# Kernel optimization log

Hardware: AMD Instinct MI355X
Metric: run time of the kernel (lower is better)

Reference implementation:

```python
import jax, jax.numpy as jnp
import numpy as np

N = 2048        # number of entities
D = 2048        # entity_dimensionality
HEADS = 16
HD = D // HEADS  # per-head dim = 128
ROUNDS = 2
LAYERS = 2


def setup_inputs() -> dict:
    key = jax.random.key(0)
    ks = jax.random.split(key, 12)
    s = 1.0 / np.sqrt(D)  # keep activations O(1)
    inp = {
        "entities": jax.random.normal(ks[0], (N, D), jnp.float32),
        "Wq": jax.random.normal(ks[1], (D, D), jnp.float32) * s,
        "bq": jnp.zeros((D,), jnp.float32),
        "Wk": jax.random.normal(ks[2], (D, D), jnp.float32) * s,
        "bk": jnp.zeros((D,), jnp.float32),
        "Wv": jax.random.normal(ks[3], (D, D), jnp.float32) * s,
        "bv": jnp.zeros((D,), jnp.float32),
        "W0": jax.random.normal(ks[4], (D, D), jnp.float32) * s,
        "b0": jnp.zeros((D,), jnp.float32),
        "W1": jax.random.normal(ks[5], (D, D), jnp.float32) * s,
        "b1": jnp.zeros((D,), jnp.float32),
    }
    return inp


def _linear(x, W, b):
    # torch nn.Linear: y = x @ W.T + b
    return x @ W.T + b


def _split_heads(x):
    # [N, D] -> [H, N, hd]
    return x.reshape(N, HEADS, HD).transpose(1, 0, 2)


def reference(entities, Wq, bq, Wk, bk, Wv, bv, W0, b0, W1, b1):
    scale = 1.0 / np.sqrt(HD)
    for _ in range(ROUNDS):
        q = _split_heads(_linear(entities, Wq, bq))  # [H, N, hd]
        k = _split_heads(_linear(entities, Wk, bk))
        v = _split_heads(_linear(entities, Wv, bv))
        scores = jnp.einsum('hqd,hkd->hqk', q, k) * scale  # [H, N, N]
        attn = jax.nn.softmax(scores, axis=-1)
        o = jnp.einsum('hqk,hkd->hqd', attn, v)            # [H, N, hd]
        o = o.transpose(1, 0, 2).reshape(N, D)             # merge heads
        o = jax.nn.relu(_linear(o, W0, b0))
        o = jax.nn.relu(_linear(o, W1, b1))
        entities = entities + o  # residual=True
    return entities
```

## Files before the change

### kernel.cpp

```cpp
#include <hip/hip_runtime.h>
#include <stdint.h>

#define DIM   2048
#define NENT  2048
#define NHEAD 16
#define HD    128

typedef unsigned short u16;
typedef u16   u16x4  __attribute__((ext_vector_type(4)));
typedef u16   u16x8  __attribute__((ext_vector_type(8)));
typedef float f32x4  __attribute__((ext_vector_type(4)));
typedef float f32x16 __attribute__((ext_vector_type(16)));
typedef __bf16 bf16x8 __attribute__((ext_vector_type(8)));

#define MFMA16(a, b, c) __builtin_amdgcn_mfma_f32_16x16x32_bf16((a), (b), (c), 0, 0, 0)
#define MFMA32(a, b, c) __builtin_amdgcn_mfma_f32_32x32x16_bf16((a), (b), (c), 0, 0, 0)

#define SMUL 0.12751743f

__device__ __forceinline__ u16 f2b(float f) {
  union { float f; unsigned int u; } x; x.f = f;
  unsigned int r = x.u + 0x7FFFu + ((x.u >> 16) & 1u);
  return (u16)(r >> 16);
}
__device__ __forceinline__ float b2f(u16 b) {
  union { unsigned int u; float f; } x; x.u = ((unsigned int)b) << 16;
  return x.f;
}
__device__ __forceinline__ unsigned int cvtpk(float a, float b) {
  unsigned int r;
  asm("v_cvt_pk_bf16_f32 %0, %1, %2" : "=v"(r) : "v"(a), "v"(b));
  return r;
}
__device__ __forceinline__ float exp2_fast(float x) {
  float r;
  asm("v_exp_f32 %0, %1" : "=v"(r) : "v"(x));
  return r;
}

__device__ __forceinline__ void async16(const void* g, void* l) {
  __builtin_amdgcn_global_load_lds(
      (const __attribute__((address_space(1))) unsigned int*)(uintptr_t)g,
      (__attribute__((address_space(3))) unsigned int*)(uintptr_t)l, 16, 0, 0);
}

__global__ void __launch_bounds__(256) conv6_k(
    const float* __restrict__ s0, const float* __restrict__ s1,
    const float* __restrict__ s2, const float* __restrict__ s3,
    const float* __restrict__ s4, const float* __restrict__ s5,
    u16* __restrict__ d0, u16* __restrict__ d1, u16* __restrict__ d2,
    u16* __restrict__ d3, u16* __restrict__ d4, u16* __restrict__ d5) {
  int sel = blockIdx.y;
  const float* s = sel == 0 ? s0 : sel == 1 ? s1 : sel == 2 ? s2
                 : sel == 3 ? s3 : sel == 4 ? s4 : s5;
  u16* d = sel == 0 ? d0 : sel == 1 ? d1 : sel == 2 ? d2
         : sel == 3 ? d3 : sel == 4 ? d4 : d5;
  int i = blockIdx.x * 256 + threadIdx.x;
  float4 v = ((const float4*)s)[i];
  u16x4 o;
  o.x = f2b(v.x); o.y = f2b(v.y); o.z = f2b(v.z); o.w = f2b(v.w);
  *(u16x4*)(d + (size_t)i * 4) = o;
}

template <int MODE, int NT>
__device__ __forceinline__ void gemm128_body(
    const u16* __restrict__ A, const u16* __restrict__ Bw,
    const float* __restrict__ bias, u16* __restrict__ C,
    int brow0, int bcol0, int kbase, float oscale) {
  __shared__ u16 lA[128 * 64];
  __shared__ u16 lB[128 * 64];
  const int tid = threadIdx.x;
  const int lane = tid & 63, w = tid >> 6;
  const int wr = w >> 1, wc = w & 1;
  const int l15 = lane & 15;
  const int koff = (lane >> 4) * 8;
  const int swz = (l15 & 7) << 3;

  f32x4 acc[4][4];
#pragma unroll
  for (int m = 0; m < 4; m++)
#pragma unroll
    for (int n = 0; n < 4; n++) acc[m][n] = (f32x4)0.f;

  const int lr = w * 8 + (lane >> 3);
  const int scol = ((lane & 7) ^ (lr & 7)) * 8;

#pragma unroll 1
  for (int kt = 0; kt < NT; kt++) {
    const int colg = kbase + kt * 64 + scol;
#pragma unroll
    for (int i = 0; i < 4; i++) {
      async16(A + (size_t)(brow0 + i * 32 + lr) * DIM + colg,
              lA + i * 2048 + w * 512);
      async16(Bw + (size_t)(bcol0 + i * 32 + lr) * DIM + colg,
              lB + i * 2048 + w * 512);
    }
    __syncthreads();
#pragma unroll
    for (int kk = 0; kk < 2; kk++) {
      bf16x8 af[4], bfr[4];
#pragma unroll
      for (int m = 0; m < 4; m++)
        af[m] = *(const bf16x8*)(lA + (wr * 64 + m * 16 + l15) * 64 +
                                 ((kk * 32 + koff) ^ swz));
#pragma unroll
      for (int n = 0; n < 4; n++)
        bfr[n] = *(const bf16x8*)(lB + (wc * 64 + n * 16 + l15) * 64 +
                                  ((kk * 32 + koff) ^ swz));
#pragma unroll
      for (int m = 0; m < 4; m++)
#pragma unroll
        for (int n = 0; n < 4; n++)
          acc[m][n] = MFMA16(af[m], bfr[n], acc[m][n]);
    }
    __syncthreads();
  }

#pragma unroll
  for (int n = 0; n < 4; n++) {
    int col = bcol0 + wc * 64 + n * 16 + l15;
    float bv = (MODE == 0) ? bias[col] : 0.f;
#pragma unroll
    for (int m = 0; m < 4; m++) {
#pragma unroll
      for (int r = 0; r < 4; r++) {
        int row = brow0 + wr * 64 + m * 16 + (lane >> 4) * 4 + r;
        float val = acc[m][n][r] + bv;
        if (MODE == 0) val *= oscale;
        C[(size_t)row * DIM + col] = f2b(val);
      }
    }
  }
}

__global__ void __launch_bounds__(256, 3) gemm128_qkv_k(
    const u16* __restrict__ A,
    const u16* __restrict__ Bq, const u16* __restrict__ Bk, const u16* __restrict__ Bv,
    const float* __restrict__ bq, const float* __restrict__ bk, const float* __restrict__ bv,
    u16* __restrict__ q, u16* __restrict__ k, u16* __restrict__ v) {
  int x = blockIdx.x & 7;
  int j = blockIdx.x >> 3;
  int bn48 = x * 6 + j % 6;
  int bm = j / 6;
  int sel = bn48 >> 4, bnn = bn48 & 15;
  const u16* B = sel == 0 ? Bq : (sel == 1 ? Bk : Bv);
  const float* bias = sel == 0 ? bq : (sel == 1 ? bk : bv);
  u16* Cc = sel == 0 ? q : (sel == 1 ? k : v);
  gemm128_body<0, 32>(A, B, bias, Cc, bm * 128, bnn * 128, 0,
                      sel == 0 ? SMUL : 1.f);
}

__global__ void __launch_bounds__(256, 3) gemm128_sk_k(
    const u16* __restrict__ A, const u16* __restrict__ Bw,
    u16* __restrict__ p0, u16* __restrict__ p1) {
  int x = blockIdx.x & 7;
  int j = blockIdx.x >> 3;
  int bn = 2 * x + (j & 1);
  int sk = (j >> 1) & 1;
  int bm = j >> 2;
  u16* part = sk ? p1 : p0;
  gemm128_body<1, 16>(A, Bw, nullptr, part, bm * 128, bn * 128, sk * 1024, 1.f);
}

template <int RESID>
__global__ void __launch_bounds__(256) reduce2_k(
    const u16* __restrict__ p0, const u16* __restrict__ p1,
    const float* __restrict__ bias, const float* __restrict__ resid,
    float* __restrict__ outf, u16* __restrict__ outb) {
  int i = blockIdx.x * 256 + threadIdx.x;
  u16x8 a0 = ((const u16x8*)p0)[i];
  u16x8 a1 = ((const u16x8*)p1)[i];
  size_t base = (size_t)i * 8;
  int col = (int)(base & (DIM - 1));
  u16x8 ob;
  float of[8];
#pragma unroll
  for (int j = 0; j < 8; j++) {
    float s = b2f(a0[j]) + b2f(a1[j]) + bias[col + j];
    s = fmaxf(s, 0.f);
    if (RESID) {
      float o = resid[base + j] + s;
      of[j] = o;
      ob[j] = f2b(o);
    } else {
      ob[j] = f2b(s);
    }
  }
  *(u16x8*)(outb + base) = ob;
  if (RESID) {
#pragma unroll
    for (int j = 0; j < 8; j++) outf[base + j] = of[j];
  }
}

__global__ void __launch_bounds__(256) transpose_v_k(const u16* __restrict__ v,
                                                     u16* __restrict__ vt) {
  __shared__ u16 t[64][72];
  int h = blockIdx.z, nb = blockIdx.y, db = blockIdx.x;
  int tid = threadIdx.x;
  int r0 = tid >> 3, c0 = (tid & 7) * 8;
#pragma unroll
  for (int p = 0; p < 2; p++) {
    int r = r0 + p * 32;
    const u16* src = v + (size_t)(nb * 64 + r) * DIM + h * HD + db * 64 + c0;
    u16x8 x = *(const u16x8*)src;
#pragma unroll
    for (int j = 0; j < 8; j++) t[r][c0 + j] = x[j];
  }
  __syncthreads();
#pragma unroll
  for (int p = 0; p < 2; p++) {
    int rr = r0 + p * 32;
    u16x8 x;
#pragma unroll
    for (int j = 0; j < 8; j++) x[j] = t[c0 + j][rr];
    *(u16x8*)(vt + (size_t)h * HD * NENT + (size_t)(db * 64 + rr) * NENT + nb * 64 + c0) = x;
  }
}

__global__ void __launch_bounds__(256, 2) attn_k(
    const u16* __restrict__ q, const u16* __restrict__ kmat,
    const u16* __restrict__ vt, u16* __restrict__ oz0, u16* __restrict__ oz1,
    float* __restrict__ ml) {
  const int h = blockIdx.x, qb = blockIdx.y, kvs = blockIdx.z;
  u16* __restrict__ oz = kvs ? oz1 : oz0;
  __shared__ u16 lK[2][64 * 128];
  __shared__ u16 lV[2][128 * 64];
  const int tid = threadIdx.x, lane = tid & 63, w = tid >> 6;
  const int l31 = lane & 31, hl = lane >> 5;
  const int r4 = lane >> 4, r8 = lane >> 3;
  const int c16e = (lane & 15) * 8, c8e = (lane & 7) * 8;
  const int swz = (l31 & 7) << 3;
  const u16* vhead = vt + (size_t)h * HD * NENT;
  const int kv0 = kvs * (NENT / 2);

  const int qrow = qb * 128 + w * 32 + l31;
  const u16* qptr = q + (size_t)qrow * DIM + h * HD + hl * 8;
  bf16x8 qf[8];
#pragma unroll
  for (int ks = 0; ks < 8; ks++)
    qf[ks] = *(const bf16x8*)(qptr + ks * 16);

  auto stageKV = [&](int kt, int buf) {
    const size_t krow0 = (size_t)kv0 + kt * 64;
#pragma unroll
    for (int c = 0; c < 4; c++) {
      int ch = w * 4 + c;
      int krow = ch * 4 + r4;
      async16(kmat + (krow0 + krow) * DIM + h * HD + (c16e ^ ((krow & 7) << 3)),
              lK[buf] + ch * 512);
      int vrow = ch * 8 + r8;
      async16(vhead + (size_t)vrow * NENT + krow0 + (c8e ^ ((r8 & 7) << 3)),
              lV[buf] + ch * 512);
    }
  };

  f32x16 Oacc[4];
#pragma unroll
  for (int dt = 0; dt < 4; dt++) Oacc[dt] = (f32x16)0.f;
  float m_i = -1e30f, l_i = 0.f;

  stageKV(0, 0);
  int cur = 0;

#pragma unroll 1
  for (int kt = 0; kt < NENT / 2 / 64; kt++) {
    __syncthreads();
    if (kt + 1 < NENT / 2 / 64) stageKV(kt + 1, cur ^ 1);
    const u16* Kc = lK[cur];
    const u16* Vc = lV[cur];

    f32x16 sA = (f32x16)0.f, sB = (f32x16)0.f;
#pragma unroll
    for (int ks = 0; ks < 8; ks++) {
      bf16x8 a0 = *(const bf16x8*)(Kc + l31 * 128 + ((ks * 16 + hl * 8) ^ swz));
      sA = MFMA32(a0, qf[ks], sA);
      bf16x8 a1 = *(const bf16x8*)(Kc + (32 + l31) * 128 + ((ks * 16 + hl * 8) ^ swz));
      sB = MFMA32(a1, qf[ks], sB);
    }

    float pmax = sA[0];
#pragma unroll
    for (int i = 1; i < 16; i++) pmax = fmaxf(pmax, sA[i]);
#pragma unroll
    for (int i = 0; i < 16; i++) pmax = fmaxf(pmax, sB[i]);
    pmax = fmaxf(pmax, __shfl_xor(pmax, 32));
    bool resc = __any(pmax > m_i + 8.f);
    float corr = 1.f;
    if (resc) {
      float mn = fmaxf(m_i, pmax);
      corr = exp2_fast(m_i - mn);
      m_i = mn;
    }
    float ls = 0.f;
#pragma unroll
    for (int i = 0; i < 16; i++) { sA[i] = exp2_fast(sA[i] - m_i); ls += sA[i]; }
#pragma unroll
    for (int i = 0; i < 16; i++) { sB[i] = exp2_fast(sB[i] - m_i); ls += sB[i]; }
    l_i = l_i * corr + ls;
    if (resc) {
#pragma unroll
      for (int r = 0; r < 16; r++) {
        int qo = hl * 4 + (r & 3) + 8 * (r >> 2);
        float cr = __shfl(corr, qo);
        Oacc[0][r] *= cr; Oacc[1][r] *= cr; Oacc[2][r] *= cr; Oacc[3][r] *= cr;
      }
    }

#pragma unroll
    for (int ks = 0; ks < 4; ks++) {
      const f32x16& p = (ks < 2) ? sA : sB;
      const int E = ((2 * ks) & 3) * 4;
      const int Od = ((2 * ks + 1) & 3) * 4;
      unsigned int e0 = cvtpk(p[E + 0], p[E + 1]);
      unsigned int e1 = cvtpk(p[E + 2], p[E + 3]);
      unsigned int o0 = cvtpk(p[Od + 0], p[Od + 1]);
      unsigned int o1 = cvtpk(p[Od + 2], p[Od + 3]);
      asm volatile("v_permlane32_swap_b32 %0, %1" : "+v"(e0), "+v"(o0));
      asm volatile("v_permlane32_swap_b32 %0, %1" : "+v"(e1), "+v"(o1));
      union { unsigned int u[4]; bf16x8 v; } pk;
      pk.u[0] = e0; pk.u[1] = e1; pk.u[2] = o0; pk.u[3] = o1;
#pragma unroll
      for (int dt = 0; dt < 4; dt++) {
        bf16x8 b = *(const bf16x8*)(Vc + (dt * 32 + l31) * 64 +
                                    ((ks * 16 + hl * 8) ^ swz));
        Oacc[dt] = MFMA32(pk.v, b, Oacc[dt]);
      }
    }
    cur ^= 1;
  }

  float lt = l_i + __shfl_xor(l_i, 32);
  if (hl == 0) {
    float* mlp = ml + ((size_t)(kvs * NHEAD + h) * NENT + qrow) * 2;
    mlp[0] = m_i;
    mlp[1] = lt;
  }
#pragma unroll
  for (int r = 0; r < 16; r++) {
    int row = qb * 128 + w * 32 + hl * 4 + (r & 3) + 8 * (r >> 2);
#pragma unroll
    for (int dt = 0; dt < 4; dt++)
      oz[(size_t)row * DIM + h * HD + dt * 32 + l31] = f2b(Oacc[dt][r]);
  }
}

__global__ void __launch_bounds__(256) combine_k(
    const u16* __restrict__ O0, const u16* __restrict__ O1,
    const float* __restrict__ ml, u16* __restrict__ o) {
  int i = blockIdx.x * 256 + threadIdx.x;
  size_t base = (size_t)i * 8;
  int row = (int)(base >> 11);
  int h = ((int)base & (DIM - 1)) >> 7;
  const float* p0 = ml + ((size_t)h * NENT + row) * 2;
  const float* p1 = ml + ((size_t)(NHEAD + h) * NENT + row) * 2;
  float m0 = p0[0], l0 = p0[1];
  float m1 = p1[0], l1 = p1[1];
  float M = fmaxf(m0, m1);
  float w0 = exp2_fast(m0 - M), w1 = exp2_fast(m1 - M);
  float inv = 1.f / (l0 * w0 + l1 * w1);
  w0 *= inv; w1 *= inv;
  u16x8 a = ((const u16x8*)O0)[i], b = ((const u16x8*)O1)[i];
  u16x8 r;
#pragma unroll
  for (int j = 0; j < 8; j++) r[j] = f2b(b2f(a[j]) * w0 + b2f(b[j]) * w1);
  ((u16x8*)o)[i] = r;
}

extern "C" void kernel_launch(void* const* d_in, const int* in_sizes, int n_in,
                              void* d_out, int out_size, void* d_ws, size_t ws_size,
                              hipStream_t stream) {
  const float* ent_in = (const float*)d_in[0];
  const float* Wq = (const float*)d_in[1];
  const float* bq = (const float*)d_in[2];
  const float* Wk = (const float*)d_in[3];
  const float* bk = (const float*)d_in[4];
  const float* Wv = (const float*)d_in[5];
  const float* bv = (const float*)d_in[6];
  const float* W0 = (const float*)d_in[7];
  const float* b0 = (const float*)d_in[8];
  const float* W1 = (const float*)d_in[9];
  const float* b1 = (const float*)d_in[10];
  float* out = (float*)d_out;

  char* ws = (char*)d_ws;
  const size_t SZ = (size_t)DIM * DIM * 2;
  u16* wqb = (u16*)ws; ws += SZ;
  u16* wkb = (u16*)ws; ws += SZ;
  u16* wvb = (u16*)ws; ws += SZ;
  u16* w0b = (u16*)ws; ws += SZ;
  u16* w1b = (u16*)ws; ws += SZ;
  u16* entb = (u16*)ws; ws += SZ;
  u16* qb_ = (u16*)ws; ws += SZ;
  u16* kb_ = (u16*)ws; ws += SZ;
  u16* vb_ = (u16*)ws; ws += SZ;
  u16* vtb = (u16*)ws; ws += SZ;
  u16* ob_ = (u16*)ws; ws += SZ;
  u16* h1b = (u16*)ws; ws += SZ;

  conv6_k<<<dim3(4096, 6), 256, 0, stream>>>(Wq, Wk, Wv, W0, W1, ent_in,
                                             wqb, wkb, wvb, w0b, w1b, entb);

  for (int r = 0; r < 2; r++) {
    const float* cur = r ? (const float*)out : ent_in;
    gemm128_qkv_k<<<768, 256, 0, stream>>>(entb, wqb, wkb, wvb, bq, bk, bv,
                                           qb_, kb_, vb_);
    transpose_v_k<<<dim3(2, 32, 16), 256, 0, stream>>>(vb_, vtb);
    attn_k<<<dim3(16, 16, 2), 256, 0, stream>>>(qb_, kb_, vtb, vb_, h1b,
                                                (float*)entb);
    combine_k<<<2048, 256, 0, stream>>>(vb_, h1b, (const float*)entb, ob_);
    gemm128_sk_k<<<512, 256, 0, stream>>>(ob_, w0b, entb, qb_);
    reduce2_k<0><<<2048, 256, 0, stream>>>(entb, qb_, b0, nullptr,
                                           nullptr, h1b);
    gemm128_sk_k<<<512, 256, 0, stream>>>(h1b, w1b, entb, qb_);
    reduce2_k<1><<<2048, 256, 0, stream>>>(entb, qb_, b1, cur,
                                           out, entb);
  }
}
```

Baseline: 365.7 us.

## Fuse V transpose into QKV GEMM epilogue and use 3-way split-K for MLP

The V projection now writes its output already transposed, staged through LDS in a swizzled per-wave arena, so the separate transpose kernel and its round trip through global memory go away. The two MLP GEMMs switch from a 2-way to a 3-way split-K (11/11/10 k-tiles, 768 blocks) to fill the CUs better, and the reduce kernel now sums three bf16 partials. The cost is one more partial buffer to read in the reduce, an extra bf16 rounding of partials, and the loop count becoming a runtime argument instead of a template constant.

```diff
diff --git a/kernel.cpp b/kernel.cpp
--- a/kernel.cpp
+++ b/kernel.cpp
@@ -62,13 +62,14 @@
   *(u16x4*)(d + (size_t)i * 4) = o;
 }
 
-template <int MODE, int NT>
+template <int MODE>
 __device__ __forceinline__ void gemm128_body(
     const u16* __restrict__ A, const u16* __restrict__ Bw,
     const float* __restrict__ bias, u16* __restrict__ C,
-    int brow0, int bcol0, int kbase, float oscale) {
-  __shared__ u16 lA[128 * 64];
-  __shared__ u16 lB[128 * 64];
+    int brow0, int bcol0, int kbase, int NT, float oscale) {
+  __shared__ u16 sbuf[2][128 * 64];
+  u16* lA = &sbuf[0][0];
+  u16* lB = &sbuf[1][0];
   const int tid = threadIdx.x;
   const int lane = tid & 63, w = tid >> 6;
   const int wr = w >> 1, wc = w & 1;
@@ -116,6 +117,36 @@
     __syncthreads();
   }
 
+  if (MODE == 2) {
+    u16* arena = &sbuf[0][0] + w * 4096;
+#pragma unroll
+    for (int n = 0; n < 4; n++) {
+      int c_loc = n * 16 + l15;
+      float bv = bias[bcol0 + wc * 64 + c_loc];
+#pragma unroll
+      for (int m = 0; m < 4; m++)
+#pragma unroll
+        for (int r = 0; r < 4; r++) {
+          int r_loc = m * 16 + (lane >> 4) * 4 + r;
+          arena[c_loc * 64 + (r_loc ^ ((c_loc & 7) * 8))] =
+              f2b(acc[m][n][r] + bv);
+        }
+    }
+    __syncthreads();
+    const int h = (bcol0 + wc * 64) >> 7;
+    const int d0 = (bcol0 + wc * 64) & 127;
+    const int R0 = brow0 + wr * 64;
+    u16* vbase = C + (size_t)h * HD * NENT + R0;
+#pragma unroll
+    for (int it = 0; it < 8; it++) {
+      int d_loc = it * 8 + (lane >> 3);
+      int r0 = (lane & 7) * 8;
+      u16x8 val = *(const u16x8*)(arena + d_loc * 64 + (r0 ^ ((d_loc & 7) * 8)));
+      *(u16x8*)(vbase + (size_t)(d0 + d_loc) * NENT + r0) = val;
+    }
+    return;
+  }
+
 #pragma unroll
   for (int n = 0; n < 4; n++) {
     int col = bcol0 + wc * 64 + n * 16 + l15;
@@ -137,46 +168,55 @@
     const u16* __restrict__ A,
     const u16* __restrict__ Bq, const u16* __restrict__ Bk, const u16* __restrict__ Bv,
     const float* __restrict__ bq, const float* __restrict__ bk, const float* __restrict__ bv,
-    u16* __restrict__ q, u16* __restrict__ k, u16* __restrict__ v) {
+    u16* __restrict__ q, u16* __restrict__ k, u16* __restrict__ vt) {
   int x = blockIdx.x & 7;
   int j = blockIdx.x >> 3;
   int bn48 = x * 6 + j % 6;
   int bm = j / 6;
   int sel = bn48 >> 4, bnn = bn48 & 15;
-  const u16* B = sel == 0 ? Bq : (sel == 1 ? Bk : Bv);
-  const float* bias = sel == 0 ? bq : (sel == 1 ? bk : bv);
-  u16* Cc = sel == 0 ? q : (sel == 1 ? k : v);
-  gemm128_body<0, 32>(A, B, bias, Cc, bm * 128, bnn * 128, 0,
-                      sel == 0 ? SMUL : 1.f);
-}
-
-__global__ void __launch_bounds__(256, 3) gemm128_sk_k(
+  if (sel == 2) {
+    gemm128_body<2>(A, Bv, bv, vt, bm * 128, bnn * 128, 0, 32, 1.f);
+  } else {
+    const u16* B = sel == 0 ? Bq : Bk;
+    const float* bias = sel == 0 ? bq : bk;
+    u16* Cc = sel == 0 ? q : k;
+    gemm128_body<0>(A, B, bias, Cc, bm * 128, bnn * 128, 0, 32,
+                    sel == 0 ? SMUL : 1.f);
+  }
+}
+
+__global__ void __launch_bounds__(256, 3) gemm128_sk3_k(
     const u16* __restrict__ A, const u16* __restrict__ Bw,
-    u16* __restrict__ p0, u16* __restrict__ p1) {
+    u16* __restrict__ p0, u16* __restrict__ p1, u16* __restrict__ p2) {
   int x = blockIdx.x & 7;
   int j = blockIdx.x >> 3;
-  int bn = 2 * x + (j & 1);
-  int sk = (j >> 1) & 1;
-  int bm = j >> 2;
-  u16* part = sk ? p1 : p0;
-  gemm128_body<1, 16>(A, Bw, nullptr, part, bm * 128, bn * 128, sk * 1024, 1.f);
+  int rem = j % 6;
+  int bn = 2 * x + (rem & 1);
+  int sk = rem >> 1;
+  int bm = j / 6;
+  u16* part = sk == 0 ? p0 : (sk == 1 ? p1 : p2);
+  int nt = (sk == 2) ? 10 : 11;
+  gemm128_body<1>(A, Bw, nullptr, part, bm * 128, bn * 128, sk * 11 * 64,
+                  nt, 1.f);
 }
 
 template <int RESID>
-__global__ void __launch_bounds__(256) reduce2_k(
+__global__ void __launch_bounds__(256) reduce3_k(
     const u16* __restrict__ p0, const u16* __restrict__ p1,
+    const u16* __restrict__ p2,
     const float* __restrict__ bias, const float* __restrict__ resid,
     float* __restrict__ outf, u16* __restrict__ outb) {
   int i = blockIdx.x * 256 + threadIdx.x;
   u16x8 a0 = ((const u16x8*)p0)[i];
   u16x8 a1 = ((const u16x8*)p1)[i];
+  u16x8 a2 = ((const u16x8*)p2)[i];
   size_t base = (size_t)i * 8;
   int col = (int)(base & (DIM - 1));
   u16x8 ob;
   float of[8];
 #pragma unroll
   for (int j = 0; j < 8; j++) {
-    float s = b2f(a0[j]) + b2f(a1[j]) + bias[col + j];
+    float s = b2f(a0[j]) + b2f(a1[j]) + b2f(a2[j]) + bias[col + j];
     s = fmaxf(s, 0.f);
     if (RESID) {
       float o = resid[base + j] + s;
@@ -190,31 +230,6 @@
   if (RESID) {
 #pragma unroll
     for (int j = 0; j < 8; j++) outf[base + j] = of[j];
-  }
-}
-
-__global__ void __launch_bounds__(256) transpose_v_k(const u16* __restrict__ v,
-                                                     u16* __restrict__ vt) {
-  __shared__ u16 t[64][72];
-  int h = blockIdx.z, nb = blockIdx.y, db = blockIdx.x;
-  int tid = threadIdx.x;
-  int r0 = tid >> 3, c0 = (tid & 7) * 8;
-#pragma unroll
-  for (int p = 0; p < 2; p++) {
-    int r = r0 + p * 32;
-    const u16* src = v + (size_t)(nb * 64 + r) * DIM + h * HD + db * 64 + c0;
-    u16x8 x = *(const u16x8*)src;
-#pragma unroll
-    for (int j = 0; j < 8; j++) t[r][c0 + j] = x[j];
-  }
-  __syncthreads();
-#pragma unroll
-  for (int p = 0; p < 2; p++) {
-    int rr = r0 + p * 32;
-    u16x8 x;
-#pragma unroll
-    for (int j = 0; j < 8; j++) x[j] = t[c0 + j][rr];
-    *(u16x8*)(vt + (size_t)h * HD * NENT + (size_t)(db * 64 + rr) * NENT + nb * 64 + c0) = x;
   }
 }
 
@@ -404,16 +419,15 @@
   for (int r = 0; r < 2; r++) {
     const float* cur = r ? (const float*)out : ent_in;
     gemm128_qkv_k<<<768, 256, 0, stream>>>(entb, wqb, wkb, wvb, bq, bk, bv,
-                                           qb_, kb_, vb_);
-    transpose_v_k<<<dim3(2, 32, 16), 256, 0, stream>>>(vb_, vtb);
+                                           qb_, kb_, vtb);
     attn_k<<<dim3(16, 16, 2), 256, 0, stream>>>(qb_, kb_, vtb, vb_, h1b,
                                                 (float*)entb);
     combine_k<<<2048, 256, 0, stream>>>(vb_, h1b, (const float*)entb, ob_);
-    gemm128_sk_k<<<512, 256, 0, stream>>>(ob_, w0b, entb, qb_);
-    reduce2_k<0><<<2048, 256, 0, stream>>>(entb, qb_, b0, nullptr,
+    gemm128_sk3_k<<<768, 256, 0, stream>>>(ob_, w0b, entb, qb_, kb_);
+    reduce3_k<0><<<2048, 256, 0, stream>>>(entb, qb_, kb_, b0, nullptr,
                                            nullptr, h1b);
-    gemm128_sk_k<<<512, 256, 0, stream>>>(h1b, w1b, entb, qb_);
-    reduce2_k<1><<<2048, 256, 0, stream>>>(entb, qb_, b1, cur,
+    gemm128_sk3_k<<<768, 256, 0, stream>>>(h1b, w1b, entb, qb_, kb_);
+    reduce3_k<1><<<2048, 256, 0, stream>>>(entb, qb_, kb_, b1, cur,
                                            out, entb);
   }
 }
```

After: 409.5 us. +12.0%, slower.
